# Kernel optimization log

Measured on AMD Instinct MI355X. Metric: run time of the kernel, lower is better.

The kernel has to match this reference:

```python
import jax, jax.numpy as jnp
from jax import lax
import numpy as np

T, D, H, E, K = 4096, 1024, 2048, 8, 2

def setup_inputs() -> dict:
    key = jax.random.key(0)
    ks = jax.random.split(key, 5)
    x = jax.random.normal(ks[0], (T, D), dtype=jnp.float32)
    weights = jax.random.uniform(ks[1], (T, K), dtype=jnp.float32)
    indices = jax.random.randint(ks[2], (T, K), 0, E, dtype=jnp.int64)
    # GatedMLP params (bias=False): fc1 weight [2H, D], fc2 weight [D, H], stacked over experts
    W1 = jax.random.normal(ks[3], (E, 2 * H, D), dtype=jnp.float32) * 0.02
    W2 = jax.random.normal(ks[4], (E, D, H), dtype=jnp.float32) * 0.02
    return {"x": x, "weights": weights, "indices": indices, "W1": W1, "W2": W2}

def reference(x, weights, indices, W1, W2):
    # Combine per-token routing weights into a per-(token, expert) weight matrix.
    # Tokens not routed to expert e get weight 0, so the dense per-expert GatedMLP
    # weighted-sum is mathematically identical to the gather->MLP->scatter-add loop.
    onehot = jax.nn.one_hot(indices, E, dtype=weights.dtype)        # [T, K, E]
    w_te = jnp.einsum('tke,tk->et', onehot, weights)                # [E, T]

    def body(y, carry):
        W1e, W2e, we = carry                                        # [2H,D], [D,H], [T]
        h = x @ W1e.T                                               # [T, 2H]
        u, gate = jnp.split(h, 2, axis=-1)                          # [T, H] each
        out = (u * jax.nn.silu(gate)) @ W2e.T                       # [T, D]
        return y + out * we[:, None], None

    y, _ = lax.scan(body, jnp.zeros_like(x), (W1, W2, w_te))
    return y
```

## Files before the change

### kernel.cpp

```cpp
#include <hip/hip_runtime.h>
#include <stdint.h>

#define T_TOK 4096
#define D_DIM 1024
#define H_DIM 2048
#define E_EXP 8
#define K_TOP 2
#define NTK   (T_TOK * K_TOP)
#define MT1 256
#define MT2 128
#define MAXT1 48
#define MAXT2 72

typedef short bf16x8 __attribute__((ext_vector_type(8)));
typedef float f32x4  __attribute__((ext_vector_type(4)));

#define MINI(a, b) ((a) < (b) ? (a) : (b))
#define MFMA_BF16 __builtin_amdgcn_mfma_f32_16x16x32_bf16

__device__ __forceinline__ unsigned short f2bf(float f) {
  unsigned u = __float_as_uint(f);
  u += 0x7fffu + ((u >> 16) & 1u);
  return (unsigned short)(u >> 16);
}

#define GLDS16(gp, lp)                                                        \
  __builtin_amdgcn_global_load_lds(                                           \
      (const __attribute__((address_space(1))) void*)(gp),                    \
      (__attribute__((address_space(3))) void*)(lp), 16, 0, 0)


#define NX8   (T_TOK * D_DIM / 8)
#define NW18  (E_EXP * 2 * H_DIM * D_DIM / 8)
#define NW28  (E_EXP * D_DIM * H_DIM / 8)
#define PRE_CVT_BLKS ((NX8 + NW18) / 256)
#define PRE_BLKS (PRE_CVT_BLKS + 32)

__global__ __launch_bounds__(256) void k_pre(const float* __restrict__ x,
                                             const float* __restrict__ W1,
                                             const int* __restrict__ idx,
                                             unsigned short* __restrict__ xb,
                                             unsigned short* __restrict__ W1b,
                                             int* __restrict__ meta) {
  int bid = blockIdx.x;
  int tid = threadIdx.x;
  if (bid >= PRE_CVT_BLKS) {
    __shared__ int h[E_EXP];
    if (tid < E_EXP) h[tid] = 0;
    __syncthreads();
    int i = (bid - PRE_CVT_BLKS) * 256 + tid;
    atomicAdd(&h[idx[i] & (E_EXP - 1)], 1);
    __syncthreads();
    if (tid < E_EXP) atomicAdd(&meta[tid], h[tid]);
    return;
  }
  long gid = (long)bid * 256 + tid;
  const float* src;
  unsigned short* dst;
  long i;
  if (gid < NX8) { src = x; dst = xb; i = gid; }
  else           { src = W1; dst = W1b; i = gid - NX8; }
  float4 a = ((const float4*)src)[2 * i];
  float4 b = ((const float4*)src)[2 * i + 1];
  uint4 o;
  o.x = f2bf(a.x) | ((unsigned)f2bf(a.y) << 16);
  o.y = f2bf(a.z) | ((unsigned)f2bf(a.w) << 16);
  o.z = f2bf(b.x) | ((unsigned)f2bf(b.y) << 16);
  o.w = f2bf(b.z) | ((unsigned)f2bf(b.w) << 16);
  ((uint4*)dst)[i] = o;
}

__global__ __launch_bounds__(256) void k_route_scatter(const int* __restrict__ idx,
                                                       const float* __restrict__ w,
                                                       int* __restrict__ meta,
                                                       unsigned short* __restrict__ rows,
                                                       unsigned short* __restrict__ slotpos,
                                                       float* __restrict__ wv) {
  __shared__ int h[E_EXP], base[E_EXP];
  int tid = threadIdx.x;
  if (tid < E_EXP) h[tid] = 0;
  __syncthreads();
  int i = blockIdx.x * 256 + tid;
  int e = idx[i] & (E_EXP - 1);
  int r = atomicAdd(&h[e], 1);
  __syncthreads();
  if (blockIdx.x == 0 && tid == 0) {
    int off = 0, nt1 = 0, nt2 = 0;
    for (int ee = 0; ee < E_EXP; ++ee) {
      int c = meta[ee];
      for (int rr = 0; rr < c; rr += MT1) {
        meta[32 + nt1]  = ee;
        meta[80 + nt1]  = off + rr;
        meta[128 + nt1] = MINI(MT1, c - rr);
        ++nt1;
      }
      for (int rr = 0; rr < c; rr += MT2) {
        meta[192 + nt2] = ee;
        meta[264 + nt2] = off + rr;
        meta[336 + nt2] = MINI(MT2, c - rr);
        ++nt2;
      }
      off += c;
    }
    meta[24] = nt1;
    meta[25] = nt2;
  }
  if (tid < E_EXP) {
    int off = 0;
#pragma unroll
    for (int ee = 0; ee < E_EXP; ++ee)
      if (ee < tid) off += meta[ee];
    base[tid] = off + atomicAdd(&meta[16 + tid], h[tid]);
  }
  __syncthreads();
  int p = base[e] + r;
  rows[p]    = (unsigned short)(i >> 1);
  slotpos[i] = (unsigned short)p;
  wv[p]      = w[i];
}

#define G1_TILES (MAXT1 * 32)
#define CVW2_BLK 1024
#define G1_GRID  (G1_TILES + CVW2_BLK)

__global__ __launch_bounds__(256, 2) void k_gemm1(
    const unsigned short* __restrict__ xb,
    const unsigned short* __restrict__ W1b,
    const int* __restrict__ meta,
    const unsigned short* __restrict__ rows,
    const float* __restrict__ wv,
    unsigned short* __restrict__ act,
    const float* __restrict__ W2,
    unsigned short* __restrict__ W2b) {
  int bid = blockIdx.x;
  int tid = threadIdx.x;

  if (bid >= G1_TILES) {
    long g0 = (long)(bid - G1_TILES) * 256 + tid;
    for (long i = g0; i < NW28; i += (long)CVW2_BLK * 256) {
      float4 a = ((const float4*)W2)[2 * i];
      float4 b = ((const float4*)W2)[2 * i + 1];
      uint4 o;
      o.x = f2bf(a.x) | ((unsigned)f2bf(a.y) << 16);
      o.y = f2bf(a.z) | ((unsigned)f2bf(a.w) << 16);
      o.z = f2bf(b.x) | ((unsigned)f2bf(b.y) << 16);
      o.w = f2bf(b.z) | ((unsigned)f2bf(b.w) << 16);
      ((uint4*)W2b)[i] = o;
    }
    return;
  }

  int nt = meta[24];
  int tb = bid % MAXT1;
  int y  = bid / MAXT1;
  if (tb >= nt) return;
  int e     = meta[32 + tb];
  int r0    = meta[80 + tb];
  int valid = meta[128 + tb];
  int n0    = y << 6;

  __shared__ unsigned short lA[256 * 64];
  __shared__ unsigned short lB1[64 * 64];
  __shared__ unsigned short lB2[64 * 64];
  __shared__ float sw[256];

  int wave = tid >> 6, lane = tid & 63;

  sw[tid] = wv[r0 + MINI(tid, valid - 1)];

  const unsigned short* w1e = W1b + (size_t)e * (4096 * 1024);

  const unsigned short *pA[8], *pB1[2], *pB2[2];
#pragma unroll
  for (int it = 0; it < 8; ++it) {
    int c = it * 256 + tid;
    int r = c >> 3, cc = c & 7;
    int g = cc ^ (r & 7);
    int tok = rows[r0 + MINI(r, valid - 1)];
    pA[it] = xb + (size_t)tok * 1024 + g * 8;
  }
#pragma unroll
  for (int it = 0; it < 2; ++it) {
    int c = it * 256 + tid;
    int r = c >> 3, cc = c & 7;
    int g = cc ^ (r & 7);
    pB1[it] = w1e + (size_t)(n0 + r) * 1024 + g * 8;
    pB2[it] = w1e + (size_t)(2048 + n0 + r) * 1024 + g * 8;
  }

  f32x4 zero = {0.f, 0.f, 0.f, 0.f};
  f32x4 au[4][4], ag[4][4];
#pragma unroll
  for (int i = 0; i < 4; ++i)
#pragma unroll
    for (int j = 0; j < 4; ++j) { au[i][j] = zero; ag[i][j] = zero; }

  int mb = wave * 64;
  int fr = lane & 15, q = lane >> 4;

  for (int k0 = 0; k0 < 1024; k0 += 64) {
    __syncthreads();
#pragma unroll
    for (int it = 0; it < 8; ++it)
      GLDS16(pA[it] + k0, &lA[(it * 256 + wave * 64) * 8]);
#pragma unroll
    for (int it = 0; it < 2; ++it) {
      int lb = (it * 256 + wave * 64) * 8;
      GLDS16(pB1[it] + k0, &lB1[lb]);
      GLDS16(pB2[it] + k0, &lB2[lb]);
    }
    __syncthreads();
#pragma unroll
    for (int kk = 0; kk < 2; ++kk) {
      int co = (((kk << 2) + q) ^ (fr & 7)) * 8 + fr * 64;
      bf16x8 a[4];
#pragma unroll
      for (int i = 0; i < 4; ++i)
        a[i] = *(const bf16x8*)&lA[(mb + i * 16) * 64 + co];
#pragma unroll
      for (int j = 0; j < 4; ++j) {
        bf16x8 bu = *(const bf16x8*)&lB1[(j * 16) * 64 + co];
        bf16x8 bg = *(const bf16x8*)&lB2[(j * 16) * 64 + co];
#pragma unroll
        for (int i = 0; i < 4; ++i) {
          au[i][j] = MFMA_BF16(a[i], bu, au[i][j], 0, 0, 0);
          ag[i][j] = MFMA_BF16(a[i], bg, ag[i][j], 0, 0, 0);
        }
      }
    }
  }

#pragma unroll
  for (int i = 0; i < 4; ++i) {
#pragma unroll
    for (int reg = 0; reg < 4; ++reg) {
      int lm = mb + i * 16 + q * 4 + reg;
      if (lm < valid) {
        float wrow = sw[lm];
        size_t orow = (size_t)(r0 + lm) * 2048;
#pragma unroll
        for (int j = 0; j < 4; ++j) {
          float u = au[i][j][reg];
          float g = ag[i][j][reg];
          float s = g / (1.f + __expf(-g));
          act[orow + (n0 + j * 16 + fr)] = f2bf(u * s * wrow);
        }
      }
    }
  }
}

#define G2_GRID (MAXT2 * 8)

__global__ __launch_bounds__(256, 2) void k_gemm2(
    const unsigned short* __restrict__ act,
    const unsigned short* __restrict__ W2b,
    const int* __restrict__ meta,
    float* __restrict__ y) {
  int bid = blockIdx.x;
  int tb = bid % MAXT2;
  int yy = bid / MAXT2;
  int nt2 = meta[25];
  if (tb >= nt2) return;
  int e     = meta[192 + tb];
  int r0    = meta[264 + tb];
  int valid = meta[336 + tb];
  int n0    = yy << 7;

  __shared__ unsigned short lA[128 * 64];
  __shared__ unsigned short lB[128 * 64];

  int tid = threadIdx.x;
  int wave = tid >> 6, lane = tid & 63;
  int wm = wave >> 1, wn = wave & 1;

  const unsigned short* w2e = W2b + (size_t)e * (1024 * 2048);

  const unsigned short *pA[4], *pB[4];
#pragma unroll
  for (int it = 0; it < 4; ++it) {
    int c = it * 256 + tid;
    int r = c >> 3, cc = c & 7;
    int g = cc ^ (r & 7);
    pA[it] = act + (size_t)(r0 + MINI(r, valid - 1)) * 2048 + g * 8;
    pB[it] = w2e + (size_t)(n0 + r) * 2048 + g * 8;
  }

  f32x4 zero = {0.f, 0.f, 0.f, 0.f};
  f32x4 acc[4][4];
#pragma unroll
  for (int i = 0; i < 4; ++i)
#pragma unroll
    for (int j = 0; j < 4; ++j) acc[i][j] = zero;

  int mb = wm * 64, nb = wn * 64;
  int fr = lane & 15, q = lane >> 4;

  for (int k0 = 0; k0 < 2048; k0 += 64) {
    __syncthreads();
#pragma unroll
    for (int it = 0; it < 4; ++it) {
      GLDS16(pA[it] + k0, &lA[(it * 256 + wave * 64) * 8]);
      GLDS16(pB[it] + k0, &lB[(it * 256 + wave * 64) * 8]);
    }
    __syncthreads();
#pragma unroll
    for (int kk = 0; kk < 2; ++kk) {
      int co = (((kk << 2) + q) ^ (fr & 7)) * 8 + fr * 64;
      bf16x8 a[4];
#pragma unroll
      for (int i = 0; i < 4; ++i)
        a[i] = *(const bf16x8*)&lA[(mb + i * 16) * 64 + co];
#pragma unroll
      for (int j = 0; j < 4; ++j) {
        bf16x8 b = *(const bf16x8*)&lB[(nb + j * 16) * 64 + co];
#pragma unroll
        for (int i = 0; i < 4; ++i)
          acc[i][j] = MFMA_BF16(a[i], b, acc[i][j], 0, 0, 0);
      }
    }
  }

#pragma unroll
  for (int i = 0; i < 4; ++i) {
#pragma unroll
    for (int reg = 0; reg < 4; ++reg) {
      int lm = mb + i * 16 + q * 4 + reg;
      if (lm < valid) {
        float* yp = y + (size_t)(r0 + lm) * 1024 + n0 + nb;
#pragma unroll
        for (int j = 0; j < 4; ++j)
          yp[j * 16 + fr] = acc[i][j][reg];
      }
    }
  }
}

__global__ __launch_bounds__(256) void k_combine(
    const float* __restrict__ y,
    const unsigned short* __restrict__ slotpos,
    float* __restrict__ out) {
  int t = blockIdx.x;
  int s0 = slotpos[2 * t], s1 = slotpos[2 * t + 1];
  const float4* a = (const float4*)(y + (size_t)s0 * 1024);
  const float4* b = (const float4*)(y + (size_t)s1 * 1024);
  float4* o = (float4*)(out + (size_t)t * 1024);
  int d = threadIdx.x;
  float4 va = a[d], vb = b[d];
  float4 vo = {va.x + vb.x, va.y + vb.y, va.z + vb.z, va.w + vb.w};
  o[d] = vo;
}

extern "C" void kernel_launch(void* const* d_in, const int* in_sizes, int n_in,
                              void* d_out, int out_size, void* d_ws, size_t ws_size,
                              hipStream_t stream) {
  const float* x  = (const float*)d_in[0];
  const float* w  = (const float*)d_in[1];
  const int*  idx = (const int*)d_in[2];
  const float* W1 = (const float*)d_in[3];
  const float* W2 = (const float*)d_in[4];
  float* out = (float*)d_out;

  char* ws = (char*)d_ws;
  unsigned short* W1b = (unsigned short*)(ws);
  float*          yslot = (float*)(ws);
  unsigned short* W2b = (unsigned short*)(ws + 67108864);
  unsigned short* xb  = (unsigned short*)(ws + 100663296);
  unsigned short* act = (unsigned short*)(ws + 109051904);
  unsigned short* rows    = (unsigned short*)(ws + 142606336);
  unsigned short* slotpos = (unsigned short*)(ws + 142622720);
  float* wv   = (float*)(ws + 142639104);
  int*   meta = (int*)(ws + 142671872);

  hipMemsetAsync(meta, 0, 2048, stream);

  k_pre<<<PRE_BLKS, 256, 0, stream>>>(x, W1, idx, xb, W1b, meta);
  k_route_scatter<<<32, 256, 0, stream>>>(idx, w, meta, rows, slotpos, wv);

  k_gemm1<<<G1_GRID, 256, 0, stream>>>(xb, W1b, meta, rows, wv, act, W2, W2b);

  k_gemm2<<<G2_GRID, 256, 0, stream>>>(act, W2b, meta, yslot);

  k_combine<<<T_TOK, 256, 0, stream>>>(yslot, slotpos, out);
}
```

Baseline: 417.4 us.

## Fuse W1 fp32-to-bf16 conversion into gemm1 B-tile loading

Removes the separate pre-pass that converts all of W1 to bf16 in workspace. gemm1 now loads fp32 W1 directly into registers, converts to bf16, and writes the swizzled tiles into LDS, replacing the async global-to-LDS loads for B. This avoids writing and re-reading a 64MB bf16 copy. In exchange, each W1 tile is read as fp32 (double the bytes) by every M-tile that uses the expert, and the synchronous register path gives up the async LDS-load overlap.

```diff
diff --git a/kernel.cpp b/kernel.cpp
--- a/kernel.cpp
+++ b/kernel.cpp
@@ -24,6 +24,10 @@
   return (unsigned short)(u >> 16);
 }
 
+__device__ __forceinline__ unsigned pk2(float lo, float hi) {
+  return (unsigned)f2bf(lo) | ((unsigned)f2bf(hi) << 16);
+}
+
 #define GLDS16(gp, lp)                                                        \
   __builtin_amdgcn_global_load_lds(                                           \
       (const __attribute__((address_space(1))) void*)(gp),                    \
@@ -31,16 +35,13 @@
 
 
 #define NX8   (T_TOK * D_DIM / 8)
-#define NW18  (E_EXP * 2 * H_DIM * D_DIM / 8)
 #define NW28  (E_EXP * D_DIM * H_DIM / 8)
-#define PRE_CVT_BLKS ((NX8 + NW18) / 256)
+#define PRE_CVT_BLKS (NX8 / 256)
 #define PRE_BLKS (PRE_CVT_BLKS + 32)
 
 __global__ __launch_bounds__(256) void k_pre(const float* __restrict__ x,
-                                             const float* __restrict__ W1,
                                              const int* __restrict__ idx,
                                              unsigned short* __restrict__ xb,
-                                             unsigned short* __restrict__ W1b,
                                              int* __restrict__ meta) {
   int bid = blockIdx.x;
   int tid = threadIdx.x;
@@ -54,20 +55,15 @@
     if (tid < E_EXP) atomicAdd(&meta[tid], h[tid]);
     return;
   }
-  long gid = (long)bid * 256 + tid;
-  const float* src;
-  unsigned short* dst;
-  long i;
-  if (gid < NX8) { src = x; dst = xb; i = gid; }
-  else           { src = W1; dst = W1b; i = gid - NX8; }
-  float4 a = ((const float4*)src)[2 * i];
-  float4 b = ((const float4*)src)[2 * i + 1];
+  long i = (long)bid * 256 + tid;
+  float4 a = ((const float4*)x)[2 * i];
+  float4 b = ((const float4*)x)[2 * i + 1];
   uint4 o;
-  o.x = f2bf(a.x) | ((unsigned)f2bf(a.y) << 16);
-  o.y = f2bf(a.z) | ((unsigned)f2bf(a.w) << 16);
-  o.z = f2bf(b.x) | ((unsigned)f2bf(b.y) << 16);
-  o.w = f2bf(b.z) | ((unsigned)f2bf(b.w) << 16);
-  ((uint4*)dst)[i] = o;
+  o.x = pk2(a.x, a.y);
+  o.y = pk2(a.z, a.w);
+  o.z = pk2(b.x, b.y);
+  o.w = pk2(b.z, b.w);
+  ((uint4*)xb)[i] = o;
 }
 
 __global__ __launch_bounds__(256) void k_route_scatter(const int* __restrict__ idx,
@@ -125,7 +121,7 @@
 
 __global__ __launch_bounds__(256, 2) void k_gemm1(
     const unsigned short* __restrict__ xb,
-    const unsigned short* __restrict__ W1b,
+    const float* __restrict__ W1f,
     const int* __restrict__ meta,
     const unsigned short* __restrict__ rows,
     const float* __restrict__ wv,
@@ -141,10 +137,10 @@
       float4 a = ((const float4*)W2)[2 * i];
       float4 b = ((const float4*)W2)[2 * i + 1];
       uint4 o;
-      o.x = f2bf(a.x) | ((unsigned)f2bf(a.y) << 16);
-      o.y = f2bf(a.z) | ((unsigned)f2bf(a.w) << 16);
-      o.z = f2bf(b.x) | ((unsigned)f2bf(b.y) << 16);
-      o.w = f2bf(b.z) | ((unsigned)f2bf(b.w) << 16);
+      o.x = pk2(a.x, a.y);
+      o.y = pk2(a.z, a.w);
+      o.z = pk2(b.x, b.y);
+      o.w = pk2(b.z, b.w);
       ((uint4*)W2b)[i] = o;
     }
     return;
@@ -168,9 +164,11 @@
 
   sw[tid] = wv[r0 + MINI(tid, valid - 1)];
 
-  const unsigned short* w1e = W1b + (size_t)e * (4096 * 1024);
-
-  const unsigned short *pA[8], *pB1[2], *pB2[2];
+  const float* w1e = W1f + (size_t)e * (4096 * 1024);
+
+  const unsigned short* pA[8];
+  const float *pBf1[2], *pBf2[2];
+  int cB[2];
 #pragma unroll
   for (int it = 0; it < 8; ++it) {
     int c = it * 256 + tid;
@@ -184,8 +182,9 @@
     int c = it * 256 + tid;
     int r = c >> 3, cc = c & 7;
     int g = cc ^ (r & 7);
-    pB1[it] = w1e + (size_t)(n0 + r) * 1024 + g * 8;
-    pB2[it] = w1e + (size_t)(2048 + n0 + r) * 1024 + g * 8;
+    cB[it] = c;
+    pBf1[it] = w1e + (size_t)(n0 + r) * 1024 + g * 8;
+    pBf2[it] = w1e + (size_t)(2048 + n0 + r) * 1024 + g * 8;
   }
 
   f32x4 zero = {0.f, 0.f, 0.f, 0.f};
@@ -200,14 +199,30 @@
 
   for (int k0 = 0; k0 < 1024; k0 += 64) {
     __syncthreads();
+    float4 bv[8];
+#pragma unroll
+    for (int it = 0; it < 2; ++it) {
+      const float4* s1 = (const float4*)(pBf1[it] + k0);
+      const float4* s2 = (const float4*)(pBf2[it] + k0);
+      bv[it * 4 + 0] = s1[0];
+      bv[it * 4 + 1] = s1[1];
+      bv[it * 4 + 2] = s2[0];
+      bv[it * 4 + 3] = s2[1];
+    }
 #pragma unroll
     for (int it = 0; it < 8; ++it)
       GLDS16(pA[it] + k0, &lA[(it * 256 + wave * 64) * 8]);
 #pragma unroll
     for (int it = 0; it < 2; ++it) {
-      int lb = (it * 256 + wave * 64) * 8;
-      GLDS16(pB1[it] + k0, &lB1[lb]);
-      GLDS16(pB2[it] + k0, &lB2[lb]);
+      uint4 o1, o2;
+      float4 u0 = bv[it * 4 + 0], u1 = bv[it * 4 + 1];
+      float4 v0 = bv[it * 4 + 2], v1 = bv[it * 4 + 3];
+      o1.x = pk2(u0.x, u0.y); o1.y = pk2(u0.z, u0.w);
+      o1.z = pk2(u1.x, u1.y); o1.w = pk2(u1.z, u1.w);
+      o2.x = pk2(v0.x, v0.y); o2.y = pk2(v0.z, v0.w);
+      o2.z = pk2(v1.x, v1.y); o2.w = pk2(v1.z, v1.w);
+      *(uint4*)&lB1[cB[it] * 8] = o1;
+      *(uint4*)&lB2[cB[it] * 8] = o2;
     }
     __syncthreads();
 #pragma unroll
@@ -362,7 +377,6 @@
   float* out = (float*)d_out;
 
   char* ws = (char*)d_ws;
-  unsigned short* W1b = (unsigned short*)(ws);
   float*          yslot = (float*)(ws);
   unsigned short* W2b = (unsigned short*)(ws + 67108864);
   unsigned short* xb  = (unsigned short*)(ws + 100663296);
@@ -374,10 +388,10 @@
 
   hipMemsetAsync(meta, 0, 2048, stream);
 
-  k_pre<<<PRE_BLKS, 256, 0, stream>>>(x, W1, idx, xb, W1b, meta);
+  k_pre<<<PRE_BLKS, 256, 0, stream>>>(x, idx, xb, meta);
   k_route_scatter<<<32, 256, 0, stream>>>(idx, w, meta, rows, slotpos, wv);
 
-  k_gemm1<<<G1_GRID, 256, 0, stream>>>(xb, W1b, meta, rows, wv, act, W2, W2b);
+  k_gemm1<<<G1_GRID, 256, 0, stream>>>(xb, W1, meta, rows, wv, act, W2, W2b);
 
   k_gemm2<<<G2_GRID, 256, 0, stream>>>(act, W2b, meta, yslot);
 
```

After: 422.3 us. No clear change (+1.2%).
